# Performance work log

Hardware: AMD Instinct MI355X
Metric: run time of the kernel (lower is better)

## Reference

```python
import jax, jax.numpy as jnp
import numpy as np

# Constants mirroring the repo enums
NUM_SPECIAL = 8
CLS = 0
CONTEXT = 1
NUM_CONTEXT = 16
NUM_BET_BINS = 16
SPECIAL_OFFSET = 52 + NUM_BET_BINS  # cards + bet bins -> 68
D_MODEL = 256
LN_EPS = 1e-5

B, S = 256, 512


def setup_inputs() -> dict:
    key = jax.random.key(0)
    ks = jax.random.split(key, 10)
    token_ids = jax.random.randint(ks[0], (B, S), 0, SPECIAL_OFFSET + NUM_SPECIAL)
    context_features = jax.random.normal(ks[1], (B, S, NUM_CONTEXT), dtype=jnp.float32)
    special_table = jax.random.normal(ks[2], (NUM_SPECIAL, D_MODEL), dtype=jnp.float32) * 0.02
    cls_w = jax.random.normal(ks[3], (3, D_MODEL), dtype=jnp.float32) * 0.1
    cls_b = jnp.zeros((D_MODEL,), jnp.float32)
    cls_ln_g = jnp.ones((D_MODEL,), jnp.float32)
    cls_ln_b = jnp.zeros((D_MODEL,), jnp.float32)
    ctx_w = jax.random.normal(ks[4], (NUM_CONTEXT, D_MODEL), dtype=jnp.float32) * 0.1
    ctx_b = jnp.zeros((D_MODEL,), jnp.float32)
    ctx_ln_g = jnp.ones((D_MODEL,), jnp.float32)
    ctx_ln_b = jnp.zeros((D_MODEL,), jnp.float32)
    return dict(token_ids=token_ids, context_features=context_features,
                special_table=special_table,
                cls_w=cls_w, cls_b=cls_b, cls_ln_g=cls_ln_g, cls_ln_b=cls_ln_b,
                ctx_w=ctx_w, ctx_b=ctx_b, ctx_ln_g=ctx_ln_g, ctx_ln_b=ctx_ln_b)


def _layernorm(x, g, b):
    mu = jnp.mean(x, axis=-1, keepdims=True)
    var = jnp.mean(jnp.square(x - mu), axis=-1, keepdims=True)
    return (x - mu) * jax.lax.rsqrt(var + LN_EPS) * g + b


def reference(token_ids, context_features, special_table,
              cls_w, cls_b, cls_ln_g, cls_ln_b,
              ctx_w, ctx_b, ctx_ln_g, ctx_ln_b):
    # Special-token embedding lookup (masked gather)
    special_ids = token_ids - SPECIAL_OFFSET
    special_mask = (token_ids >= SPECIAL_OFFSET) & (token_ids < SPECIAL_OFFSET + NUM_SPECIAL)
    safe_ids = jnp.clip(special_ids, 0, NUM_SPECIAL - 1)
    emb = jnp.where(special_mask[..., None], special_table[safe_ids], 0.0)  # [B,S,D]

    # CLS branch: Linear(3->D) -> LayerNorm -> ReLU (dropout is identity in eval)
    cls_mask = token_ids == SPECIAL_OFFSET + CLS
    cls_h = jax.nn.relu(_layernorm(context_features[..., :3] @ cls_w + cls_b, cls_ln_g, cls_ln_b))
    emb = emb + jnp.where(cls_mask[..., None], cls_h, 0.0)

    # CONTEXT branch: Linear(NUM_CONTEXT->D) -> LayerNorm -> ReLU
    ctx_mask = token_ids == SPECIAL_OFFSET + CONTEXT
    ctx_h = jax.nn.relu(_layernorm(context_features @ ctx_w + ctx_b, ctx_ln_g, ctx_ln_b))
    emb = emb + jnp.where(ctx_mask[..., None], ctx_h, 0.0)
    return emb
```

## Files before the change

kernel.cpp:

```cpp
#include <hip/hip_runtime.h>

#define D_MODEL 256
#define SPECIAL_OFFSET 68
#define NUM_SPECIAL 8
#define NUM_CONTEXT 16
#define LN_EPS 1e-5f

typedef float f32x4 __attribute__((ext_vector_type(4)));

__global__ __launch_bounds__(256) void ctx_emb_kernel(
    const int*   __restrict__ token_ids,
    const float* __restrict__ context_features,
    const float* __restrict__ special_table,
    const float* __restrict__ cls_w,
    const float* __restrict__ cls_b,
    const float* __restrict__ cls_g,
    const float* __restrict__ cls_be,
    const float* __restrict__ ctx_w,
    const float* __restrict__ ctx_b,
    const float* __restrict__ ctx_g,
    const float* __restrict__ ctx_be,
    float*       __restrict__ out,
    int n_tokens)
{
    const int lane  = threadIdx.x & 63;
    const int wave0 = (int)((blockIdx.x * (unsigned)blockDim.x + threadIdx.x) >> 6);
    const int W     = (int)((gridDim.x * (unsigned)blockDim.x) >> 6);
    const int d0    = lane * 4;

    for (int tok = wave0; tok < n_tokens; tok += W) {
        const int tid = token_ids[tok];

        f32x4 acc = {0.f, 0.f, 0.f, 0.f};

        if (tid >= SPECIAL_OFFSET && tid < SPECIAL_OFFSET + NUM_SPECIAL) {
            acc = *(const f32x4*)(special_table + (tid - SPECIAL_OFFSET) * D_MODEL + d0);
        }

        const bool is_cls = (tid == SPECIAL_OFFSET);
        const bool is_ctx = (tid == SPECIAL_OFFSET + 1);

        if (is_cls || is_ctx) {
            const float* w  = is_cls ? cls_w  : ctx_w;
            const float* bb = is_cls ? cls_b  : ctx_b;
            const float* g  = is_cls ? cls_g  : ctx_g;
            const float* be = is_cls ? cls_be : ctx_be;
            const int    K  = is_cls ? 3 : NUM_CONTEXT;

            const float* f = context_features + (size_t)tok * NUM_CONTEXT;

            f32x4 h = *(const f32x4*)(bb + d0);
            for (int k = 0; k < K; ++k) {
                const float fk = f[k];
                const f32x4 wk = *(const f32x4*)(w + k * D_MODEL + d0);
                h.x = fmaf(fk, wk.x, h.x);
                h.y = fmaf(fk, wk.y, h.y);
                h.z = fmaf(fk, wk.z, h.z);
                h.w = fmaf(fk, wk.w, h.w);
            }

            float s  = h.x + h.y + h.z + h.w;
            float sq = h.x * h.x + h.y * h.y + h.z * h.z + h.w * h.w;
            #pragma unroll
            for (int m = 1; m < 64; m <<= 1) {
                s  += __shfl_xor(s,  m, 64);
                sq += __shfl_xor(sq, m, 64);
            }
            const float mu  = s * (1.0f / D_MODEL);
            const float var = sq * (1.0f / D_MODEL) - mu * mu;
            const float rs  = rsqrtf(var + LN_EPS);

            const f32x4 gv = *(const f32x4*)(g  + d0);
            const f32x4 bv = *(const f32x4*)(be + d0);
            acc.x += fmaxf((h.x - mu) * rs * gv.x + bv.x, 0.f);
            acc.y += fmaxf((h.y - mu) * rs * gv.y + bv.y, 0.f);
            acc.z += fmaxf((h.z - mu) * rs * gv.z + bv.z, 0.f);
            acc.w += fmaxf((h.w - mu) * rs * gv.w + bv.w, 0.f);
        }

        *(f32x4*)(out + (size_t)tok * D_MODEL + d0) = acc;
    }
}

extern "C" void kernel_launch(void* const* d_in, const int* in_sizes, int n_in,
                              void* d_out, int out_size, void* d_ws, size_t ws_size,
                              hipStream_t stream) {
    const int*   token_ids = (const int*)  d_in[0];
    const float* ctx_feat  = (const float*)d_in[1];
    const float* special   = (const float*)d_in[2];
    const float* cls_w     = (const float*)d_in[3];
    const float* cls_b     = (const float*)d_in[4];
    const float* cls_g     = (const float*)d_in[5];
    const float* cls_be    = (const float*)d_in[6];
    const float* ctx_w     = (const float*)d_in[7];
    const float* ctx_b     = (const float*)d_in[8];
    const float* ctx_g     = (const float*)d_in[9];
    const float* ctx_be    = (const float*)d_in[10];
    float*       out       = (float*)d_out;

    const int n_tokens = in_sizes[0];
    const int grid = 2048;

    ctx_emb_kernel<<<grid, 256, 0, stream>>>(
        token_ids, ctx_feat, special,
        cls_w, cls_b, cls_g, cls_be,
        ctx_w, ctx_b, ctx_g, ctx_be,
        out, n_tokens);
}
```

Measured before the change: 31.60 us.

## Split into bulk zero-fill kernel and sparse special-token row kernel

A dedicated vectorized zero-fill kernel now clears the whole output. A second kernel reads one token id per lane, uses a wave ballot to find special tokens, and writes only those rows: the table lookup plus the CLS/CONTEXT linear-LayerNorm-ReLU. The aim is to make the dominant traffic a plain streaming store with no per-token id loads or branching. In exchange it adds a second launch and rewrites roughly a tenth of the rows, so some output bytes are written twice.

```diff
diff --git a/kernel.cpp b/kernel.cpp
--- a/kernel.cpp
+++ b/kernel.cpp
@@ -8,7 +8,18 @@
 
 typedef float f32x4 __attribute__((ext_vector_type(4)));
 
-__global__ __launch_bounds__(256) void ctx_emb_kernel(
+__global__ __launch_bounds__(256) void fill_zero_kernel(float* __restrict__ out,
+                                                        long n_f32x4)
+{
+    const long tid0   = (long)blockIdx.x * blockDim.x + threadIdx.x;
+    const long stride = (long)gridDim.x * blockDim.x;
+    f32x4* p = (f32x4*)out;
+    const f32x4 z = {0.f, 0.f, 0.f, 0.f};
+    for (long i = tid0; i < n_f32x4; i += stride)
+        p[i] = z;
+}
+
+__global__ __launch_bounds__(256) void special_rows_kernel(
     const int*   __restrict__ token_ids,
     const float* __restrict__ context_features,
     const float* __restrict__ special_table,
@@ -23,19 +34,26 @@
     float*       __restrict__ out,
     int n_tokens)
 {
-    const int lane  = threadIdx.x & 63;
-    const int wave0 = (int)((blockIdx.x * (unsigned)blockDim.x + threadIdx.x) >> 6);
-    const int W     = (int)((gridDim.x * (unsigned)blockDim.x) >> 6);
-    const int d0    = lane * 4;
+    const int lane = threadIdx.x & 63;
+    const int wave = (int)((blockIdx.x * (unsigned)blockDim.x + threadIdx.x) >> 6);
+    const int base = wave * 64;
+    if (base >= n_tokens) return;
 
-    for (int tok = wave0; tok < n_tokens; tok += W) {
-        const int tid = token_ids[tok];
+    const int my_tok = base + lane;
+    const int my_tid = (my_tok < n_tokens) ? token_ids[my_tok] : 0;
+    const bool my_special = (my_tid >= SPECIAL_OFFSET) &&
+                            (my_tid <  SPECIAL_OFFSET + NUM_SPECIAL);
 
-        f32x4 acc = {0.f, 0.f, 0.f, 0.f};
+    unsigned long long m = __ballot(my_special);
+    const int d0 = lane * 4;
 
-        if (tid >= SPECIAL_OFFSET && tid < SPECIAL_OFFSET + NUM_SPECIAL) {
-            acc = *(const f32x4*)(special_table + (tid - SPECIAL_OFFSET) * D_MODEL + d0);
-        }
+    while (m) {
+        const int t = __ffsll((long long)m) - 1;
+        m &= m - 1;
+        const int tid = __shfl(my_tid, t, 64);
+        const int tok = base + t;
+
+        f32x4 acc = *(const f32x4*)(special_table + (tid - SPECIAL_OFFSET) * D_MODEL + d0);
 
         const bool is_cls = (tid == SPECIAL_OFFSET);
         const bool is_ctx = (tid == SPECIAL_OFFSET + 1);
@@ -62,9 +80,9 @@
             float s  = h.x + h.y + h.z + h.w;
             float sq = h.x * h.x + h.y * h.y + h.z * h.z + h.w * h.w;
             #pragma unroll
-            for (int m = 1; m < 64; m <<= 1) {
-                s  += __shfl_xor(s,  m, 64);
-                sq += __shfl_xor(sq, m, 64);
+            for (int mm = 1; mm < 64; mm <<= 1) {
+                s  += __shfl_xor(s,  mm, 64);
+                sq += __shfl_xor(sq, mm, 64);
             }
             const float mu  = s * (1.0f / D_MODEL);
             const float var = sq * (1.0f / D_MODEL) - mu * mu;
@@ -99,9 +117,13 @@
     float*       out       = (float*)d_out;
 
     const int n_tokens = in_sizes[0];
-    const int grid = 2048;
 
-    ctx_emb_kernel<<<grid, 256, 0, stream>>>(
+    const long n_f32x4 = (long)out_size / 4;
+    fill_zero_kernel<<<2048, 256, 0, stream>>>(out, n_f32x4);
+
+    const int tokens_per_block = 4 * 64;
+    const int gridB = (n_tokens + tokens_per_block - 1) / tokens_per_block;
+    special_rows_kernel<<<gridB, 256, 0, stream>>>(
         token_ids, ctx_feat, special,
         cls_w, cls_b, cls_g, cls_be,
         ctx_w, ctx_b, ctx_g, ctx_be,
```

Measured after the change: 48.16 us. 52.4% more time.
